# Kernel tuning notes

Measured on AMD Instinct MI355X. Metric: run time of the kernel, lower is better.

## Reference

```python
import jax, jax.numpy as jnp
import numpy as np

B, T, D_IN, H, N_CLASSES = 32, 64, 10000, 200, 2


def setup_inputs() -> dict:
    key = jax.random.key(0)
    ks = jax.random.split(key, 16)
    s_in = 1.0 / np.sqrt(H)  # torch nn.RNN init scale
    def u(k, shape):
        return jax.random.uniform(k, shape, jnp.float32, -s_in, s_in)
    inp = {"x": jax.random.normal(ks[0], (B, T, D_IN), jnp.float32)}
    dims = [D_IN, H, H]
    for l in range(3):
        inp[f"W_ih{l}"] = u(ks[1 + 4 * l], (H, dims[l]))
        inp[f"W_hh{l}"] = u(ks[2 + 4 * l], (H, H))
        inp[f"b_ih{l}"] = u(ks[3 + 4 * l], (H,))
        inp[f"b_hh{l}"] = u(ks[4 + 4 * l], (H,))
    inp["fc_w"] = u(ks[13], (N_CLASSES, H))
    inp["fc_b"] = u(ks[14], (N_CLASSES,))
    return inp


def _rnn_layer(x_seq, W_ih, W_hh, b_ih, b_hh):
    # x_seq: [B, T, D] -> hidden sequence [B, T, H]
    pre = jnp.einsum('btd,hd->bth', x_seq, W_ih) + b_ih + b_hh  # input proj batched over time
    h0 = jnp.zeros((x_seq.shape[0], W_hh.shape[0]), x_seq.dtype)

    def step(h, p_t):
        h_new = jnp.tanh(p_t + h @ W_hh.T)
        return h_new, h_new

    _, hs = jax.lax.scan(step, h0, jnp.swapaxes(pre, 0, 1))  # [T, B, H]
    return jnp.swapaxes(hs, 0, 1)


def reference(x, W_ih0, W_hh0, b_ih0, b_hh0, W_ih1, W_hh1, b_ih1, b_hh1,
              W_ih2, W_hh2, b_ih2, b_hh2, fc_w, fc_b):
    h = _rnn_layer(x, W_ih0, W_hh0, b_ih0, b_hh0)
    h = _rnn_layer(h, W_ih1, W_hh1, b_ih1, b_hh1)
    h = _rnn_layer(h, W_ih2, W_hh2, b_ih2, b_hh2)
    last = h[:, -1, :]  # [B, H]; dropout is identity at inference
    logits = last @ fc_w.T + fc_b  # [B, n_classes]
    return logits
```

## Files before the change

kernel.cpp:

```cpp
#include <hip/hip_runtime.h>
#include <hip/hip_bf16.h>


typedef __bf16  bf16x8 __attribute__((ext_vector_type(8)));
typedef __bf16  bf16x4 __attribute__((ext_vector_type(4)));
typedef float   f32x4  __attribute__((ext_vector_type(4)));

#define HDIM 200
#define BM 64
#define CHUNK_B 26624
#define MFMA(a, b, c) __builtin_amdgcn_mfma_f32_16x16x32_bf16(a, b, c, 0, 0, 0)

__device__ __forceinline__ void glds16(const void* g, void* l) {
    __builtin_amdgcn_global_load_lds(
        (const __attribute__((address_space(1))) unsigned int*)g,
        (__attribute__((address_space(3))) unsigned int*)l, 16, 0, 0);
}

__device__ __forceinline__ float fast_tanh(float x) {
    float e = __expf(-2.f * fabsf(x));
    float r = (1.f - e) / (1.f + e);
    return copysignf(r, x);
}

__device__ __forceinline__ void bar_lds() {
    asm volatile("s_waitcnt lgkmcnt(0)" ::: "memory");
    __builtin_amdgcn_s_barrier();
}

__global__ void pack_all(const float* __restrict__ W0,
                         const float* __restrict__ W1,
                         const float* __restrict__ W2,
                         __bf16* __restrict__ O0,
                         __bf16* __restrict__ O1,
                         __bf16* __restrict__ O2)
{
    const int T0 = 320 * 1664, T1 = 7 * 1664, T2 = 7 * 1664;
    for (int gt = blockIdx.x * blockDim.x + threadIdx.x; gt < T0 + T1 + T2;
         gt += gridDim.x * blockDim.x) {
        const float* W; __bf16* out; int K, g;
        if (gt < T0)           { W = W0; out = O0; K = 10000; g = gt; }
        else if (gt < T0 + T1) { W = W1; out = O1; K = HDIM;  g = gt - T0; }
        else                   { W = W2; out = O2; K = HDIM;  g = gt - T0 - T1; }

        const int kc = g / 1664;
        const int u  = g - kc * 1664;
        const int isLo = (u >= 832);
        const int u2 = isLo ? u - 832 : u;
        const int nt = u2 >> 6;
        const int l  = u2 & 63;
        const int r  = nt * 16 + (l & 15);
        const int k  = kc * 32 + (l >> 4) * 8;
        bf16x8 v;
        if (r < HDIM && k < K) {
            const float* p = W + (size_t)r * K + k;
            float4 a = *(const float4*)p, b = *(const float4*)(p + 4);
            float f[8] = {a.x, a.y, a.z, a.w, b.x, b.y, b.z, b.w};
#pragma unroll
            for (int i = 0; i < 8; ++i) {
                __bf16 h = (__bf16)f[i];
                v[i] = isLo ? (__bf16)(f[i] - (float)h) : h;
            }
        } else {
#pragma unroll
            for (int i = 0; i < 8; ++i) v[i] = (__bf16)0.f;
        }
        *(bf16x8*)&out[(size_t)g * 8] = v;
    }
}

__device__ __noinline__ void gemm_job(
    const float* __restrict__ A, int lda, int K,
    const __bf16* __restrict__ Bpack, float* __restrict__ C,
    int ksteps, int kc0, int m0,
    __bf16* Ab, __bf16* Bb, int tid)
{
    const int wv = tid >> 6, lane = tid & 63;
    const int r16 = lane & 15, kg = lane >> 4;
    const int mg = wv & 1, ng = wv >> 1;
    const int nt0 = ng ? 1 + ng * 3 : 0;
    const int ntw = ng ? 3 : 4;
    const int fb  = lane * 8;

    const int a_row = tid >> 3;
    const int a_q   = tid & 7;
    const float* Arow = A + (size_t)(m0 + a_row) * lda + a_q * 4;
    const int a_off = (a_row >> 4) * 512 + ((a_row & 15) + 16 * (a_q >> 1)) * 8
                    + (a_q & 1) * 4;

    f32x4 acc[2][4];
#pragma unroll
    for (int mi = 0; mi < 2; ++mi)
#pragma unroll
        for (int j = 0; j < 4; ++j) acc[mi][j] = (f32x4)0.f;

    float av[4];
    auto loadA = [&](int ks) {
        const int kb = (kc0 + ks) * 32;
        if (kb + a_q * 4 < K) {
            float4 x0 = *(const float4*)(Arow + kb);
            av[0] = x0.x; av[1] = x0.y; av[2] = x0.z; av[3] = x0.w;
        } else {
#pragma unroll
            for (int i = 0; i < 4; ++i) av[i] = 0.f;
        }
    };
    auto issueB = [&](int ks, int buf) {
        const char* src = (const char*)Bpack + (size_t)(kc0 + ks) * CHUNK_B;
        char* dst = (char*)Bb + (size_t)buf * CHUNK_B;
#pragma unroll
        for (int r = 0; r < 3; ++r)
            glds16(src + (r * 512 + tid) * 16, dst + (r * 512 + tid) * 16);
        if (tid < 128)
            glds16(src + (1536 + tid) * 16, dst + (1536 + tid) * 16);
    };

    loadA(0);
    issueB(0, 0);

    for (int ks = 0; ks < ksteps; ++ks) {
        const int cur = ks & 1, nxt = cur ^ 1;
        bf16x4 th, tl;
#pragma unroll
        for (int i = 0; i < 4; ++i) {
            __bf16 h = (__bf16)av[i];
            th[i] = h; tl[i] = (__bf16)(av[i] - (float)h);
        }
        *(bf16x4*)&Ab[cur * 4096 + a_off]        = th;
        *(bf16x4*)&Ab[cur * 4096 + 2048 + a_off] = tl;
        __syncthreads();
        if (ks + 1 < ksteps) { issueB(ks + 1, nxt); loadA(ks + 1); }

        const int ao0 = (mg * 2 + 0) * 512 + fb;
        const int ao1 = (mg * 2 + 1) * 512 + fb;
        bf16x8 ah0 = *(const bf16x8*)&Ab[cur * 4096 + ao0];
        bf16x8 al0 = *(const bf16x8*)&Ab[cur * 4096 + 2048 + ao0];
        bf16x8 ah1 = *(const bf16x8*)&Ab[cur * 4096 + ao1];
        bf16x8 al1 = *(const bf16x8*)&Ab[cur * 4096 + 2048 + ao1];
#pragma unroll
        for (int j = 0; j < 4; ++j) {
            if (j < ntw) {
                const int bo = (nt0 + j) * 512 + fb;
                bf16x8 bh = *(const bf16x8*)&Bb[cur * 13312 + bo];
                bf16x8 bl = *(const bf16x8*)&Bb[cur * 13312 + 6656 + bo];
                acc[0][j] = MFMA(al0, bh, acc[0][j]);
                acc[0][j] = MFMA(ah0, bl, acc[0][j]);
                acc[0][j] = MFMA(ah0, bh, acc[0][j]);
                acc[1][j] = MFMA(al1, bh, acc[1][j]);
                acc[1][j] = MFMA(ah1, bl, acc[1][j]);
                acc[1][j] = MFMA(ah1, bh, acc[1][j]);
            }
        }
    }

#pragma unroll
    for (int mi = 0; mi < 2; ++mi) {
        const int rb = m0 + mg * 32 + mi * 16 + kg * 4;
#pragma unroll
        for (int j = 0; j < 4; ++j) {
            if (j < ntw) {
                const int n = (nt0 + j) * 16 + r16;
                if (n < HDIM)
#pragma unroll
                    for (int r = 0; r < 4; ++r)
                        C[(size_t)(rb + r) * HDIM + n] = acc[mi][j][r];
            }
        }
    }
    __syncthreads();
}

__global__ __launch_bounds__(512, 4)
void gemm_l0(const float* __restrict__ x, const __bf16* __restrict__ W0p,
             float* __restrict__ Ppart, int per_split)
{
    __shared__ alignas(16) char U[69632];
    gemm_job(x, 10000, 10000, W0p,
             Ppart + (size_t)blockIdx.y * per_split,
             20, blockIdx.y * 20, blockIdx.x * BM,
             (__bf16*)U, (__bf16*)(U + 16384), threadIdx.x);
}

__global__ void reduce_parts(const float* __restrict__ Pp, float* __restrict__ P)
{
    const int i = blockIdx.x * blockDim.x + threadIdx.x;
    if (i < 102400) {
        float4 s = ((const float4*)Pp)[i];
#pragma unroll
        for (int r = 1; r < 16; ++r) {
            float4 v = ((const float4*)Pp)[(size_t)r * 102400 + i];
            s.x += v.x; s.y += v.y; s.z += v.z; s.w += v.w;
        }
        ((float4*)P)[i] = s;
    }
}

__global__ __launch_bounds__(512, 1)
void rnn_chain(float* P, float* Hbuf,
               const float* __restrict__ Whh0, const float* __restrict__ bih0,
               const float* __restrict__ bhh0,
               const float* __restrict__ Whh1, const float* __restrict__ bih1,
               const float* __restrict__ bhh1,
               const float* __restrict__ Whh2, const float* __restrict__ bih2,
               const float* __restrict__ bhh2,
               const __bf16* __restrict__ W1p, const __bf16* __restrict__ W2p,
               const float* __restrict__ fcw, const float* __restrict__ fcb,
               float* __restrict__ outp)
{
    const int b   = blockIdx.x;
    const int tid = threadIdx.x;

    __shared__ alignas(16) char U[69632];
    __bf16* Ab   = (__bf16*)U;
    __bf16* Bb   = (__bf16*)(U + 16384);
    float*  preS = (float*)U;
    float*  hS   = (float*)(U + 51200);
    float*  bias = (float*)(U + 52000);
    float*  part = (float*)(U + 52800);

    auto rec = [&](const float* pre, const float* Whh, const float* bih,
                   const float* bhh, float* Hout) {
        {
            const float4* ps = (const float4*)(pre + (size_t)b * 64 * HDIM);
            float4* pd = (float4*)preS;
            for (int i = tid; i < 3200; i += 512) pd[i] = ps[i];
        }

        const bool act = tid < 500;
        const int g  = tid / 10;
        const int s  = tid - g * 10;
        const int n0 = g * 4;
        const int k0 = s * 20;

        float w[80];
        if (act) {
#pragma unroll
            for (int j = 0; j < 4; ++j) {
                const float* wr = Whh + (size_t)(n0 + j) * HDIM + k0;
#pragma unroll
                for (int i = 0; i < 5; ++i) {
                    float4 v = *(const float4*)(wr + i * 4);
                    w[j * 20 + i * 4 + 0] = v.x; w[j * 20 + i * 4 + 1] = v.y;
                    w[j * 20 + i * 4 + 2] = v.z; w[j * 20 + i * 4 + 3] = v.w;
                }
            }
        }
        if (tid < HDIM) { bias[tid] = bih[tid] + bhh[tid]; hS[tid] = 0.f; }
        __syncthreads();

        for (int t = 0; t < 64; ++t) {
            if (act) {
                float a0 = 0.f, a1 = 0.f, a2 = 0.f, a3 = 0.f;
#pragma unroll
                for (int i = 0; i < 5; ++i) {
                    float4 hv = *(const float4*)&hS[k0 + i * 4];
                    a0 += w[ 0 + i*4]*hv.x + w[ 1 + i*4]*hv.y + w[ 2 + i*4]*hv.z + w[ 3 + i*4]*hv.w;
                    a1 += w[20 + i*4]*hv.x + w[21 + i*4]*hv.y + w[22 + i*4]*hv.z + w[23 + i*4]*hv.w;
                    a2 += w[40 + i*4]*hv.x + w[41 + i*4]*hv.y + w[42 + i*4]*hv.z + w[43 + i*4]*hv.w;
                    a3 += w[60 + i*4]*hv.x + w[61 + i*4]*hv.y + w[62 + i*4]*hv.z + w[63 + i*4]*hv.w;
                }
                float4 pv = make_float4(a0, a1, a2, a3);
                *(float4*)&part[s * HDIM + n0] = pv;
            }
            bar_lds();
            if (tid < HDIM) {
                float sum = part[0 * HDIM + tid];
#pragma unroll
                for (int r = 1; r < 10; ++r) sum += part[r * HDIM + tid];
                float v = fast_tanh(sum + preS[t * HDIM + tid] + bias[tid]);
                hS[tid] = v;
                Hout[((size_t)b * 64 + t) * HDIM + tid] = v;
            }
            bar_lds();
        }
    };

    float* Hslab = Hbuf + (size_t)b * 64 * HDIM;
    float* Pslab = P + (size_t)b * 64 * HDIM;

    rec(P, Whh0, bih0, bhh0, Hbuf);
    __syncthreads();
    gemm_job(Hslab, HDIM, HDIM, W1p, Pslab, 7, 0, 0, Ab, Bb, tid);

    rec(P, Whh1, bih1, bhh1, Hbuf);
    __syncthreads();
    gemm_job(Hslab, HDIM, HDIM, W2p, Pslab, 7, 0, 0, Ab, Bb, tid);

    rec(P, Whh2, bih2, bhh2, Hbuf);

    if (tid < 16) {
        const int cls = tid & 1, sl = tid >> 1;
        const float* fw = fcw + cls * HDIM + sl * 25;
        const float* hp = hS + sl * 25;
        float sacc = 0.f;
#pragma unroll
        for (int j = 0; j < 25; ++j) sacc += hp[j] * fw[j];
        sacc += __shfl_xor(sacc, 2);
        sacc += __shfl_xor(sacc, 4);
        sacc += __shfl_xor(sacc, 8);
        if (sl == 0) outp[b * 2 + cls] = sacc + fcb[cls];
    }
}

extern "C" void kernel_launch(void* const* d_in, const int* in_sizes, int n_in,
                              void* d_out, int out_size, void* d_ws, size_t ws_size,
                              hipStream_t stream) {
    const float* x     = (const float*)d_in[0];
    const float* W_ih0 = (const float*)d_in[1];
    const float* W_hh0 = (const float*)d_in[2];
    const float* b_ih0 = (const float*)d_in[3];
    const float* b_hh0 = (const float*)d_in[4];
    const float* W_ih1 = (const float*)d_in[5];
    const float* W_hh1 = (const float*)d_in[6];
    const float* b_ih1 = (const float*)d_in[7];
    const float* b_hh1 = (const float*)d_in[8];
    const float* W_ih2 = (const float*)d_in[9];
    const float* W_hh2 = (const float*)d_in[10];
    const float* b_ih2 = (const float*)d_in[11];
    const float* b_hh2 = (const float*)d_in[12];
    const float* fc_w  = (const float*)d_in[13];
    const float* fc_b  = (const float*)d_in[14];
    float* out = (float*)d_out;

    const size_t PE = (size_t)2048 * HDIM;
    float* P     = (float*)d_ws;
    float* Hbuf  = P + PE;
    float* Ppart = Hbuf + PE;
    __bf16* W0p  = (__bf16*)(Ppart + 16 * PE);
    __bf16* W1p  = W0p + (size_t)320 * 13312;
    __bf16* W2p  = W1p + (size_t)7 * 13312;

    pack_all<<<1024, 256, 0, stream>>>(W_ih0, W_ih1, W_ih2, W0p, W1p, W2p);
    gemm_l0<<<dim3(32, 16), 512, 0, stream>>>(x, W0p, Ppart, (int)PE);
    reduce_parts<<<400, 256, 0, stream>>>(Ppart, P);
    rnn_chain<<<32, 512, 0, stream>>>(P, Hbuf,
                                      W_hh0, b_ih0, b_hh0,
                                      W_hh1, b_ih1, b_hh1,
                                      W_hh2, b_ih2, b_hh2,
                                      W1p, W2p, fc_w, fc_b, out);
}
```

Baseline: 329.0 us.

## Run recurrent matvec on MFMA with split-bf16 weights and fuse partial-sum reduction

The per-timestep recurrent h@W_hh product moves from scalar FP32 FMAs with a cross-thread partial reduction to bf16 MFMA instructions. Weights are packed as hi/lo bf16 pairs and kept in registers, and h is stored in LDS as hi/lo bf16. This removes the 10-way LDS partial-sum reduction pass on every step. The separate reduce_parts kernel is also dropped, and the 16-way split-K sum is folded into the rnn_chain preload, which saves one launch and one round trip of the pre-activation buffer through global memory. In exchange, 14 of 16 rows of each MFMA tile are wasted, precision depends on the three-term split-bf16 scheme, and the 32 blocks now read all 16 partial buffers serially.

After: 431.4 us. 1.31x slower.

```diff
diff --git a/kernel.cpp b/kernel.cpp
--- a/kernel.cpp
+++ b/kernel.cpp
@@ -28,20 +28,36 @@
     __builtin_amdgcn_s_barrier();
 }
 
-__global__ void pack_all(const float* __restrict__ W0,
-                         const float* __restrict__ W1,
-                         const float* __restrict__ W2,
-                         __bf16* __restrict__ O0,
-                         __bf16* __restrict__ O1,
-                         __bf16* __restrict__ O2)
+__global__ void pack_all(const float* __restrict__ Wi0,
+                         const float* __restrict__ Wi1,
+                         const float* __restrict__ Wi2,
+                         const float* __restrict__ Wh0,
+                         const float* __restrict__ Wh1,
+                         const float* __restrict__ Wh2,
+                         __bf16* __restrict__ Oi0,
+                         __bf16* __restrict__ Oi1,
+                         __bf16* __restrict__ Oi2,
+                         __bf16* __restrict__ Oh0,
+                         __bf16* __restrict__ Oh1,
+                         __bf16* __restrict__ Oh2)
 {
-    const int T0 = 320 * 1664, T1 = 7 * 1664, T2 = 7 * 1664;
-    for (int gt = blockIdx.x * blockDim.x + threadIdx.x; gt < T0 + T1 + T2;
+    const int T0 = 320 * 1664, TS = 7 * 1664;
+    const int total = T0 + 5 * TS;
+    for (int gt = blockIdx.x * blockDim.x + threadIdx.x; gt < total;
          gt += gridDim.x * blockDim.x) {
         const float* W; __bf16* out; int K, g;
-        if (gt < T0)           { W = W0; out = O0; K = 10000; g = gt; }
-        else if (gt < T0 + T1) { W = W1; out = O1; K = HDIM;  g = gt - T0; }
-        else                   { W = W2; out = O2; K = HDIM;  g = gt - T0 - T1; }
+        if (gt < T0)               { W = Wi0; out = Oi0; K = 10000; g = gt; }
+        else {
+            int r5 = gt - T0;
+            int which = r5 / TS;   g = r5 - which * TS;  K = HDIM;
+            switch (which) {
+                case 0: W = Wi1; out = Oi1; break;
+                case 1: W = Wi2; out = Oi2; break;
+                case 2: W = Wh0; out = Oh0; break;
+                case 3: W = Wh1; out = Oh1; break;
+                default: W = Wh2; out = Oh2; break;
+            }
+        }
 
         const int kc = g / 1664;
         const int u  = g - kc * 1664;
@@ -181,27 +197,14 @@
              (__bf16*)U, (__bf16*)(U + 16384), threadIdx.x);
 }
 
-__global__ void reduce_parts(const float* __restrict__ Pp, float* __restrict__ P)
-{
-    const int i = blockIdx.x * blockDim.x + threadIdx.x;
-    if (i < 102400) {
-        float4 s = ((const float4*)Pp)[i];
-#pragma unroll
-        for (int r = 1; r < 16; ++r) {
-            float4 v = ((const float4*)Pp)[(size_t)r * 102400 + i];
-            s.x += v.x; s.y += v.y; s.z += v.z; s.w += v.w;
-        }
-        ((float4*)P)[i] = s;
-    }
-}
-
 __global__ __launch_bounds__(512, 1)
-void rnn_chain(float* P, float* Hbuf,
-               const float* __restrict__ Whh0, const float* __restrict__ bih0,
+void rnn_chain(const float* __restrict__ Ppart, int nparts, int pstride,
+               float* P, float* Hbuf,
+               const __bf16* __restrict__ Wh0p, const float* __restrict__ bih0,
                const float* __restrict__ bhh0,
-               const float* __restrict__ Whh1, const float* __restrict__ bih1,
+               const __bf16* __restrict__ Wh1p, const float* __restrict__ bih1,
                const float* __restrict__ bhh1,
-               const float* __restrict__ Whh2, const float* __restrict__ bih2,
+               const __bf16* __restrict__ Wh2p, const float* __restrict__ bih2,
                const float* __restrict__ bhh2,
                const __bf16* __restrict__ W1p, const __bf16* __restrict__ W2p,
                const float* __restrict__ fcw, const float* __restrict__ fcb,
@@ -214,62 +217,87 @@
     __bf16* Ab   = (__bf16*)U;
     __bf16* Bb   = (__bf16*)(U + 16384);
     float*  preS = (float*)U;
-    float*  hS   = (float*)(U + 51200);
-    float*  bias = (float*)(U + 52000);
-    float*  part = (float*)(U + 52800);
-
-    auto rec = [&](const float* pre, const float* Whh, const float* bih,
-                   const float* bhh, float* Hout) {
+    float*  bias = (float*)(U + 51200);
+    float*  hF   = (float*)(U + 52000);
+    __bf16* hSh  = (__bf16*)(U + 52800);
+    __bf16* hSl  = (__bf16*)(U + 53264);
+
+    const int wv = tid >> 6, lane = tid & 63;
+    const int kg = lane >> 4;
+    const int ntA = wv;
+    const int ntB = wv + 8;
+
+    auto recM = [&](const float* preG, int np, int pstr,
+                    const __bf16* WhhP, const float* bih, const float* bhh,
+                    float* Hout) {
         {
-            const float4* ps = (const float4*)(pre + (size_t)b * 64 * HDIM);
+            const float4* ps = (const float4*)(preG + (size_t)b * 64 * HDIM);
             float4* pd = (float4*)preS;
-            for (int i = tid; i < 3200; i += 512) pd[i] = ps[i];
-        }
-
-        const bool act = tid < 500;
-        const int g  = tid / 10;
-        const int s  = tid - g * 10;
-        const int n0 = g * 4;
-        const int k0 = s * 20;
-
-        float w[80];
-        if (act) {
-#pragma unroll
-            for (int j = 0; j < 4; ++j) {
-                const float* wr = Whh + (size_t)(n0 + j) * HDIM + k0;
-#pragma unroll
-                for (int i = 0; i < 5; ++i) {
-                    float4 v = *(const float4*)(wr + i * 4);
-                    w[j * 20 + i * 4 + 0] = v.x; w[j * 20 + i * 4 + 1] = v.y;
-                    w[j * 20 + i * 4 + 2] = v.z; w[j * 20 + i * 4 + 3] = v.w;
+            const size_t pq = (size_t)pstr / 4;
+            for (int i = tid; i < 3200; i += 512) {
+                float4 s = ps[i];
+                for (int r = 1; r < np; ++r) {
+                    float4 v = ps[(size_t)r * pq + i];
+                    s.x += v.x; s.y += v.y; s.z += v.z; s.w += v.w;
                 }
-            }
-        }
-        if (tid < HDIM) { bias[tid] = bih[tid] + bhh[tid]; hS[tid] = 0.f; }
+                pd[i] = s;
+            }
+        }
+        if (tid < HDIM) bias[tid] = bih[tid] + bhh[tid];
+        if (tid < 224) { hSh[tid] = (__bf16)0.f; hSl[tid] = (__bf16)0.f; }
+
+        bf16x8 wA[7][2], wB[7][2];
+#pragma unroll
+        for (int kc = 0; kc < 7; ++kc) {
+            const __bf16* s0 = WhhP + (size_t)kc * 13312 + ((size_t)ntA * 64 + lane) * 8;
+            wA[kc][0] = *(const bf16x8*)s0;
+            wA[kc][1] = *(const bf16x8*)(s0 + 6656);
+            if (ntB < 13) {
+                const __bf16* s1 = WhhP + (size_t)kc * 13312 + ((size_t)ntB * 64 + lane) * 8;
+                wB[kc][0] = *(const bf16x8*)s1;
+                wB[kc][1] = *(const bf16x8*)(s1 + 6656);
+            } else {
+#pragma unroll
+                for (int i = 0; i < 8; ++i) { wB[kc][0][i] = (__bf16)0.f; wB[kc][1][i] = (__bf16)0.f; }
+            }
+        }
         __syncthreads();
 
         for (int t = 0; t < 64; ++t) {
-            if (act) {
-                float a0 = 0.f, a1 = 0.f, a2 = 0.f, a3 = 0.f;
-#pragma unroll
-                for (int i = 0; i < 5; ++i) {
-                    float4 hv = *(const float4*)&hS[k0 + i * 4];
-                    a0 += w[ 0 + i*4]*hv.x + w[ 1 + i*4]*hv.y + w[ 2 + i*4]*hv.z + w[ 3 + i*4]*hv.w;
-                    a1 += w[20 + i*4]*hv.x + w[21 + i*4]*hv.y + w[22 + i*4]*hv.z + w[23 + i*4]*hv.w;
-                    a2 += w[40 + i*4]*hv.x + w[41 + i*4]*hv.y + w[42 + i*4]*hv.z + w[43 + i*4]*hv.w;
-                    a3 += w[60 + i*4]*hv.x + w[61 + i*4]*hv.y + w[62 + i*4]*hv.z + w[63 + i*4]*hv.w;
+            bf16x8 hh[7], hl[7];
+#pragma unroll
+            for (int kc = 0; kc < 7; ++kc) {
+                hh[kc] = *(const bf16x8*)&hSh[kc * 32 + kg * 8];
+                hl[kc] = *(const bf16x8*)&hSl[kc * 32 + kg * 8];
+            }
+            f32x4 aA = (f32x4)0.f, aB = (f32x4)0.f;
+#pragma unroll
+            for (int kc = 0; kc < 7; ++kc) {
+                aA = MFMA(hl[kc], wA[kc][0], aA);
+                aA = MFMA(hh[kc], wA[kc][1], aA);
+                aA = MFMA(hh[kc], wA[kc][0], aA);
+                aB = MFMA(hl[kc], wB[kc][0], aB);
+                aB = MFMA(hh[kc], wB[kc][1], aB);
+                aB = MFMA(hh[kc], wB[kc][0], aB);
+            }
+            bar_lds();
+            if (lane < 16) {
+                {
+                    const int n = ntA * 16 + lane;
+                    float v = fast_tanh(aA[0] + preS[t * HDIM + n] + bias[n]);
+                    __bf16 vh = (__bf16)v;
+                    hSh[n] = vh; hSl[n] = (__bf16)(v - (float)vh);
+                    hF[n] = v;
+                    Hout[((size_t)b * 64 + t) * HDIM + n] = v;
                 }
-                float4 pv = make_float4(a0, a1, a2, a3);
-                *(float4*)&part[s * HDIM + n0] = pv;
-            }
-            bar_lds();
-            if (tid < HDIM) {
-                float sum = part[0 * HDIM + tid];
-#pragma unroll
-                for (int r = 1; r < 10; ++r) sum += part[r * HDIM + tid];
-                float v = fast_tanh(sum + preS[t * HDIM + tid] + bias[tid]);
-                hS[tid] = v;
-                Hout[((size_t)b * 64 + t) * HDIM + tid] = v;
+                const int n = ntB * 16 + lane;
+                if (n < HDIM) {
+                    float v = fast_tanh(aB[0] + preS[t * HDIM + n] + bias[n]);
+                    __bf16 vh = (__bf16)v;
+                    hSh[n] = vh; hSl[n] = (__bf16)(v - (float)vh);
+                    hF[n] = v;
+                    Hout[((size_t)b * 64 + t) * HDIM + n] = v;
+                }
             }
             bar_lds();
         }
@@ -278,20 +306,20 @@
     float* Hslab = Hbuf + (size_t)b * 64 * HDIM;
     float* Pslab = P + (size_t)b * 64 * HDIM;
 
-    rec(P, Whh0, bih0, bhh0, Hbuf);
+    recM(Ppart, nparts, pstride, Wh0p, bih0, bhh0, Hbuf);
     __syncthreads();
     gemm_job(Hslab, HDIM, HDIM, W1p, Pslab, 7, 0, 0, Ab, Bb, tid);
 
-    rec(P, Whh1, bih1, bhh1, Hbuf);
+    recM(P, 1, 0, Wh1p, bih1, bhh1, Hbuf);
     __syncthreads();
     gemm_job(Hslab, HDIM, HDIM, W2p, Pslab, 7, 0, 0, Ab, Bb, tid);
 
-    rec(P, Whh2, bih2, bhh2, Hbuf);
+    recM(P, 1, 0, Wh2p, bih2, bhh2, Hbuf);
 
     if (tid < 16) {
         const int cls = tid & 1, sl = tid >> 1;
         const float* fw = fcw + cls * HDIM + sl * 25;
-        const float* hp = hS + sl * 25;
+        const float* hp = hF + sl * 25;
         float sacc = 0.f;
 #pragma unroll
         for (int j = 0; j < 25; ++j) sacc += hp[j] * fw[j];
@@ -323,19 +351,24 @@
     float* out = (float*)d_out;
 
     const size_t PE = (size_t)2048 * HDIM;
+    const size_t CH = (size_t)7 * 13312;
     float* P     = (float*)d_ws;
     float* Hbuf  = P + PE;
     float* Ppart = Hbuf + PE;
     __bf16* W0p  = (__bf16*)(Ppart + 16 * PE);
     __bf16* W1p  = W0p + (size_t)320 * 13312;
-    __bf16* W2p  = W1p + (size_t)7 * 13312;
-
-    pack_all<<<1024, 256, 0, stream>>>(W_ih0, W_ih1, W_ih2, W0p, W1p, W2p);
+    __bf16* W2p  = W1p + CH;
+    __bf16* Wh0p = W2p + CH;
+    __bf16* Wh1p = Wh0p + CH;
+    __bf16* Wh2p = Wh1p + CH;
+
+    pack_all<<<1024, 256, 0, stream>>>(W_ih0, W_ih1, W_ih2,
+                                       W_hh0, W_hh1, W_hh2,
+                                       W0p, W1p, W2p, Wh0p, Wh1p, Wh2p);
     gemm_l0<<<dim3(32, 16), 512, 0, stream>>>(x, W0p, Ppart, (int)PE);
-    reduce_parts<<<400, 256, 0, stream>>>(Ppart, P);
-    rnn_chain<<<32, 512, 0, stream>>>(P, Hbuf,
-                                      W_hh0, b_ih0, b_hh0,
-                                      W_hh1, b_ih1, b_hh1,
-                                      W_hh2, b_ih2, b_hh2,
+    rnn_chain<<<32, 512, 0, stream>>>(Ppart, 16, (int)PE, P, Hbuf,
+                                      Wh0p, b_ih0, b_hh0,
+                                      Wh1p, b_ih1, b_hh1,
+                                      Wh2p, b_ih2, b_hh2,
                                       W1p, W2p, fc_w, fc_b, out);
 }
```
